# Kernel tuning notes

Measured on AMD Instinct MI355X. Metric: run time of the kernel, lower is better.

## Reference

```python
import jax, jax.numpy as jnp
import numpy as np

N_NODES = 100000
N_EDGES = 1600000
IN_CH = 128
HID = 128
OUT_CH = 64
NUM_GRAPHS = 64


def glorot(key, shape):
    lim = float(np.sqrt(6.0 / (shape[0] + shape[1])))
    return jax.random.uniform(key, shape, jnp.float32, -lim, lim)


def setup_inputs() -> dict:
    key = jax.random.key(0)
    ks = jax.random.split(key, 12)
    x = jax.random.normal(ks[0], (N_NODES, IN_CH), jnp.float32)
    edge_index = jax.random.randint(ks[1], (2, N_EDGES), 0, N_NODES, jnp.int64)
    batch = jax.random.randint(ks[2], (N_NODES,), 0, NUM_GRAPHS, jnp.int64)
    return {
        "x": x,
        "edge_index": edge_index,
        "batch": batch,
        "W1": glorot(ks[3], (IN_CH, HID)), "b1": jnp.zeros((HID,), jnp.float32),
        "W2": glorot(ks[4], (HID, HID)), "b2": jnp.zeros((HID,), jnp.float32),
        "W3": glorot(ks[5], (HID, HID)), "b3": jnp.zeros((HID,), jnp.float32),
        "Wp": glorot(ks[6], (HID, OUT_CH)), "bp": jnp.zeros((OUT_CH,), jnp.float32),
    }


def gcn_conv(x, W, b, src, dst, norm_edge, self_norm):
    # h = X W + b ; out = scatter_add(norm * h[src] -> dst) + self_loop term
    h = x @ W + b
    msg = h[src] * norm_edge[:, None]            # [E, d]
    agg = jax.ops.segment_sum(msg, dst, num_segments=N_NODES)
    return agg + h * self_norm[:, None]


def reference(x, edge_index, batch, W1, b1, W2, b2, W3, b3, Wp, bp):
    src, dst = edge_index[0], edge_index[1]
    # symmetric normalization with self-loops: deg = in-degree + 1
    deg = jax.ops.segment_sum(jnp.ones((N_EDGES,), x.dtype), dst, num_segments=N_NODES) + 1.0
    dinv = jax.lax.rsqrt(deg)
    norm_edge = dinv[src] * dinv[dst]            # [E]
    self_norm = dinv * dinv                      # [N] (self-loop weight)

    h = jax.nn.relu(gcn_conv(x, W1, b1, src, dst, norm_edge, self_norm))
    h = jax.nn.relu(gcn_conv(h, W2, b2, src, dst, norm_edge, self_norm))
    h = gcn_conv(h, W3, b3, src, dst, norm_edge, self_norm)

    # global mean pool over graphs
    sums = jax.ops.segment_sum(h, batch, num_segments=NUM_GRAPHS)
    counts = jax.ops.segment_sum(jnp.ones((N_NODES,), h.dtype), batch, num_segments=NUM_GRAPHS)
    pooled = sums / jnp.maximum(counts, 1.0)[:, None]   # [G, HID]
    return pooled @ Wp + bp                               # [G, OUT_CH]
```

## Files before the change

kernel.cpp:

```cpp
#include <hip/hip_runtime.h>

#define N_NODES 100000
#define N_EDGES 1600000
#define CH      128
#define OUT_CH  64
#define NUM_G   64
#define NREP    8

typedef unsigned short ushort_t;
typedef unsigned int uint_t;
typedef __attribute__((ext_vector_type(8))) short short8;
typedef __attribute__((ext_vector_type(4))) float f32x4;

#define WB 64
#define EB 6250
#define EB8 782
#define GB ((N_NODES + 63) / 64)
#define GB2 ((N_NODES + 127) / 128)
#define AB ((N_NODES + 3) / 4)
#define SB 98

__device__ __forceinline__ ushort_t f2b(float f) {
    union { float f; uint_t i; } v; v.f = f;
    uint_t u = v.i;
    uint_t r = (u + 0x7fffu + ((u >> 16) & 1u)) >> 16;
    return (ushort_t)r;
}
__device__ __forceinline__ float blo(uint_t u) {
    union { uint_t i; float f; } v; v.i = u << 16; return v.f;
}
__device__ __forceinline__ float bhi(uint_t u) {
    union { uint_t i; float f; } v; v.i = u & 0xffff0000u; return v.f;
}

__global__ __launch_bounds__(256) void prep_kernel(const float* __restrict__ W1,
                                                   const float* __restrict__ W2,
                                                   const float* __restrict__ W3,
                                                   ushort_t* __restrict__ Wt1,
                                                   ushort_t* __restrict__ Wt2,
                                                   ushort_t* __restrict__ Wt3,
                                                   const int* __restrict__ dst,
                                                   int* __restrict__ cnt8,
                                                   int* __restrict__ pos) {
    int b = blockIdx.x, tid = threadIdx.x;
    if (b < EB) {
        int e = b * 256 + tid;
        if (e < N_EDGES) {
            int r = b & (NREP - 1);
            pos[e] = atomicAdd(&cnt8[(size_t)r * N_NODES + dst[e]], 1);
        }
    } else {
        int wi = (b - EB) / WB;
        const float* W  = (wi == 0) ? W1 : (wi == 1) ? W2 : W3;
        ushort_t*   Wt = (wi == 0) ? Wt1 : (wi == 1) ? Wt2 : Wt3;
        int t = ((b - EB) % WB) * 256 + tid;
        int k = t >> 7, n = t & 127;
        Wt[(size_t)n * CH + k] = f2b(W[t]);
    }
}

__device__ __forceinline__ int wave_incl_scan(int v, int lane) {
#pragma unroll
    for (int off = 1; off < 64; off <<= 1) {
        int t = __shfl_up(v, off);
        if (lane >= off) v += t;
    }
    return v;
}

__global__ __launch_bounds__(1024) void scan_p1(int* __restrict__ cnt8,
                                                int* __restrict__ ptr,
                                                int* __restrict__ bsum,
                                                float* __restrict__ dinv,
                                                const int* __restrict__ batch,
                                                int* __restrict__ counts) {
    __shared__ int s_w[16];
    __shared__ int s_c[NUM_G];
    int tid = threadIdx.x, lane = tid & 63, wid = tid >> 6;
    int i = blockIdx.x * 1024 + tid;
    int v = 0;
    if (i < N_NODES) {
        int run = 0;
#pragma unroll
        for (int r = 0; r < NREP; ++r) {
            size_t idx = (size_t)r * N_NODES + i;
            int t = cnt8[idx];
            cnt8[idx] = run;
            run += t;
        }
        v = run;
        dinv[i] = rsqrtf((float)v + 1.0f);
    }
    int incl = wave_incl_scan(v, lane);
    if (lane == 63) s_w[wid] = incl;
    if (tid < NUM_G) s_c[tid] = 0;
    __syncthreads();
    if (tid < 16) {
        int w = s_w[tid];
#pragma unroll
        for (int off = 1; off < 16; off <<= 1) {
            int t = __shfl_up(w, off);
            if (tid >= off) w += t;
        }
        s_w[tid] = w;
    }
    if (i < N_NODES) atomicAdd(&s_c[batch[i]], 1);
    __syncthreads();
    int woff = (wid > 0) ? s_w[wid - 1] : 0;
    if (i < N_NODES) ptr[i] = woff + incl - v;
    if (tid == 0) bsum[blockIdx.x] = s_w[15];
    if (tid < NUM_G) atomicAdd(&counts[tid], s_c[tid]);
}

__global__ __launch_bounds__(128) void scan_p2(const int* __restrict__ bsum,
                                               int* __restrict__ boff,
                                               int* __restrict__ ptr) {
    __shared__ int s_w[2];
    int tid = threadIdx.x, lane = tid & 63, wid = tid >> 6;
    int v = (tid < SB) ? bsum[tid] : 0;
    int incl = wave_incl_scan(v, lane);
    if (lane == 63) s_w[wid] = incl;
    __syncthreads();
    int woff = (wid == 1) ? s_w[0] : 0;
    int excl = woff + incl - v;
    if (tid < SB) boff[tid] = excl;
    if (tid == SB - 1) ptr[N_NODES] = excl + v;
}

__global__ __launch_bounds__(1024) void scan_p3(int* __restrict__ ptr,
                                                const int* __restrict__ boff,
                                                int* __restrict__ cnt8) {
    int i = blockIdx.x * 1024 + threadIdx.x;
    if (i < N_NODES) {
        int fp = ptr[i] + boff[blockIdx.x];
        ptr[i] = fp;
#pragma unroll
        for (int r = 0; r < NREP; ++r)
            cnt8[(size_t)r * N_NODES + i] += fp;
    }
}

template <bool F32A>
__device__ __forceinline__ void gemm_body(int bid, int tid,
                                          const void* __restrict__ A,
                                          const ushort_t* __restrict__ Wt,
                                          const float* __restrict__ bias,
                                          ushort_t* __restrict__ H) {
    int wv = tid >> 6, lane = tid & 63;
    int q = lane >> 4, ml = lane & 15;
    int r0 = bid * 64 + wv * 16;
    int arow = r0 + ml;
    if (arow >= N_NODES) arow = N_NODES - 1;

    f32x4 acc[8];
#pragma unroll
    for (int ct = 0; ct < 8; ++ct) { acc[ct][0] = 0.f; acc[ct][1] = 0.f; acc[ct][2] = 0.f; acc[ct][3] = 0.f; }

#pragma unroll
    for (int ks = 0; ks < 4; ++ks) {
        short8 af;
        if constexpr (F32A) {
            const float* ap = (const float*)A + (size_t)arow * CH + ks * 32 + q * 8;
            f32x4 v0 = *(const f32x4*)ap;
            f32x4 v1 = *(const f32x4*)(ap + 4);
#pragma unroll
            for (int j = 0; j < 4; ++j) {
                af[j]     = (short)f2b(v0[j]);
                af[j + 4] = (short)f2b(v1[j]);
            }
        } else {
            const ushort_t* ap = (const ushort_t*)A + (size_t)arow * CH + ks * 32 + q * 8;
            af = *(const short8*)ap;
        }
#pragma unroll
        for (int ct = 0; ct < 8; ++ct) {
            short8 bf = *(const short8*)(Wt + (size_t)(ct * 16 + ml) * CH + ks * 32 + q * 8);
            acc[ct] = __builtin_amdgcn_mfma_f32_16x16x32_bf16(af, bf, acc[ct], 0, 0, 0);
        }
    }

#pragma unroll
    for (int ct = 0; ct < 8; ++ct) {
        int col = ct * 16 + ml;
        float bv = bias[col];
#pragma unroll
        for (int i = 0; i < 4; ++i) {
            int rr = r0 + q * 4 + i;
            if (rr < N_NODES)
                H[(size_t)rr * CH + col] = f2b(acc[ct][i] + bv);
        }
    }
}

__global__ __launch_bounds__(256) void fill_gemm1(const int* __restrict__ src,
                                                  const int* __restrict__ dst,
                                                  const int* __restrict__ pos,
                                                  const int* __restrict__ cnt8,
                                                  int* __restrict__ csr_src,
                                                  const float* __restrict__ x,
                                                  const ushort_t* __restrict__ Wt,
                                                  const float* __restrict__ bias,
                                                  ushort_t* __restrict__ H) {
    if (blockIdx.x < EB8) {
        int e = (blockIdx.x * 256 + threadIdx.x) * 8;
        if (e < N_EDGES) {
            const int* base = cnt8 + (size_t)((e >> 8) & (NREP - 1)) * N_NODES;
            int4 da = *(const int4*)(dst + e);
            int4 db = *(const int4*)(dst + e + 4);
            int4 pa = *(const int4*)(pos + e);
            int4 pb = *(const int4*)(pos + e + 4);
            int4 sa = *(const int4*)(src + e);
            int4 sb = *(const int4*)(src + e + 4);
            csr_src[base[da.x] + pa.x] = sa.x;
            csr_src[base[da.y] + pa.y] = sa.y;
            csr_src[base[da.z] + pa.z] = sa.z;
            csr_src[base[da.w] + pa.w] = sa.w;
            csr_src[base[db.x] + pb.x] = sb.x;
            csr_src[base[db.y] + pb.y] = sb.y;
            csr_src[base[db.z] + pb.z] = sb.z;
            csr_src[base[db.w] + pb.w] = sb.w;
        }
    } else {
        gemm_body<true>(blockIdx.x - EB8, threadIdx.x, x, Wt, bias, H);
    }
}

__global__ __launch_bounds__(512) void gemm_mfma(const ushort_t* __restrict__ A,
                                                 const ushort_t* __restrict__ Wt,
                                                 const float* __restrict__ bias,
                                                 ushort_t* __restrict__ H) {
    __shared__ ushort_t sW[CH * CH];
    int tid = threadIdx.x;
    for (int i = tid; i < CH * CH / 8; i += 512) {
        int row = i >> 4, slot = i & 15;
        uint4 v = *(const uint4*)(Wt + (size_t)row * CH + slot * 8);
        *(uint4*)(&sW[row * CH + ((slot ^ (row & 7)) * 8)]) = v;
    }
    __syncthreads();

    int wv = tid >> 6, lane = tid & 63;
    int q = lane >> 4, ml = lane & 15;
    int r0 = blockIdx.x * 128 + wv * 16;
    int arow = r0 + ml;
    if (arow >= N_NODES) arow = N_NODES - 1;
    const ushort_t* ap = A + (size_t)arow * CH;

    f32x4 acc[8];
#pragma unroll
    for (int ct = 0; ct < 8; ++ct) { acc[ct][0] = 0.f; acc[ct][1] = 0.f; acc[ct][2] = 0.f; acc[ct][3] = 0.f; }

#pragma unroll
    for (int ks = 0; ks < 4; ++ks) {
        short8 af = *(const short8*)(ap + ks * 32 + q * 8);
        int slot = ks * 4 + q;
#pragma unroll
        for (int ct = 0; ct < 8; ++ct) {
            int srow = ct * 16 + ml;
            short8 bf = *(const short8*)(&sW[srow * CH + ((slot ^ (srow & 7)) * 8)]);
            acc[ct] = __builtin_amdgcn_mfma_f32_16x16x32_bf16(af, bf, acc[ct], 0, 0, 0);
        }
    }

#pragma unroll
    for (int ct = 0; ct < 8; ++ct) {
        int col = ct * 16 + ml;
        float bv = bias[col];
#pragma unroll
        for (int i = 0; i < 4; ++i) {
            int rr = r0 + q * 4 + i;
            if (rr < N_NODES)
                H[(size_t)rr * CH + col] = f2b(acc[ct][i] + bv);
        }
    }
}

__device__ __forceinline__ void agg_node(int node, int lane, int q, int c8,
                                         const ushort_t* __restrict__ h,
                                         const int* __restrict__ csr_src,
                                         const int* __restrict__ ptr,
                                         const float* __restrict__ dinv,
                                         float (&acc)[8]) {
    int beg = ptr[node], end = ptr[node + 1];
#pragma unroll
    for (int i = 0; i < 8; ++i) acc[i] = 0.0f;

    for (int e0 = beg; e0 < end; e0 += 64) {
        int e = e0 + lane;
        int s = 0; float w = 0.0f;
        if (e < end) { s = csr_src[e]; w = dinv[s]; }
        int m = min(64, end - e0);
        for (int j0 = 0; j0 < m; j0 += 4) {
            int   sj = __shfl(s, j0 + q);
            float wj = __shfl(w, j0 + q);
            uint4 u = *(const uint4*)(h + (size_t)sj * CH + c8);
            acc[0] = fmaf(wj, blo(u.x), acc[0]);
            acc[1] = fmaf(wj, bhi(u.x), acc[1]);
            acc[2] = fmaf(wj, blo(u.y), acc[2]);
            acc[3] = fmaf(wj, bhi(u.y), acc[3]);
            acc[4] = fmaf(wj, blo(u.z), acc[4]);
            acc[5] = fmaf(wj, bhi(u.z), acc[5]);
            acc[6] = fmaf(wj, blo(u.w), acc[6]);
            acc[7] = fmaf(wj, bhi(u.w), acc[7]);
        }
    }

#pragma unroll
    for (int i = 0; i < 8; ++i) {
        acc[i] += __shfl_xor(acc[i], 16);
        acc[i] += __shfl_xor(acc[i], 32);
    }

    float dn = dinv[node];
    uint4 us = *(const uint4*)(h + (size_t)node * CH + c8);
    acc[0] = dn * fmaf(dn, blo(us.x), acc[0]);
    acc[1] = dn * fmaf(dn, bhi(us.x), acc[1]);
    acc[2] = dn * fmaf(dn, blo(us.y), acc[2]);
    acc[3] = dn * fmaf(dn, bhi(us.y), acc[3]);
    acc[4] = dn * fmaf(dn, blo(us.z), acc[4]);
    acc[5] = dn * fmaf(dn, bhi(us.z), acc[5]);
    acc[6] = dn * fmaf(dn, blo(us.w), acc[6]);
    acc[7] = dn * fmaf(dn, bhi(us.w), acc[7]);
}

__global__ __launch_bounds__(256) void agg_bf16(const ushort_t* __restrict__ h,
                                                const int* __restrict__ csr_src,
                                                const int* __restrict__ ptr,
                                                const float* __restrict__ dinv,
                                                ushort_t* __restrict__ outp) {
    int wv = threadIdx.x >> 6, lane = threadIdx.x & 63;
    int node = blockIdx.x * 4 + wv;
    if (node >= N_NODES) return;
    int q = lane >> 4;
    int c8 = (lane & 15) * 8;

    float acc[8];
    agg_node(node, lane, q, c8, h, csr_src, ptr, dinv, acc);

#pragma unroll
    for (int i = 0; i < 8; ++i) acc[i] = fmaxf(acc[i], 0.0f);

    if (q == 0) {
        uint4 o;
        o.x = (uint_t)f2b(acc[0]) | ((uint_t)f2b(acc[1]) << 16);
        o.y = (uint_t)f2b(acc[2]) | ((uint_t)f2b(acc[3]) << 16);
        o.z = (uint_t)f2b(acc[4]) | ((uint_t)f2b(acc[5]) << 16);
        o.w = (uint_t)f2b(acc[6]) | ((uint_t)f2b(acc[7]) << 16);
        *(uint4*)(outp + (size_t)node * CH + c8) = o;
    }
}

__global__ __launch_bounds__(256) void agg_pool(const ushort_t* __restrict__ h,
                                                const int* __restrict__ csr_src,
                                                const int* __restrict__ ptr,
                                                const float* __restrict__ dinv,
                                                const int* __restrict__ batch,
                                                float* __restrict__ gsums) {
    int wv = threadIdx.x >> 6, lane = threadIdx.x & 63;
    int node = blockIdx.x * 4 + wv;
    if (node >= N_NODES) return;
    int q = lane >> 4;
    int c8 = (lane & 15) * 8;

    float acc[8];
    agg_node(node, lane, q, c8, h, csr_src, ptr, dinv, acc);

    int g = batch[node];
    int jb = q * 2;
    float* bp = gsums + (size_t)(blockIdx.x & (NREP - 1)) * (NUM_G * CH)
                      + g * CH + c8 + jb;
    unsafeAtomicAdd(&bp[0], acc[jb]);
    unsafeAtomicAdd(&bp[1], acc[jb + 1]);
}

__global__ __launch_bounds__(128) void out_kernel(const float* __restrict__ gsums,
                                                  const int* __restrict__ counts,
                                                  const float* __restrict__ Wp,
                                                  const float* __restrict__ bp,
                                                  float* __restrict__ outp) {
    __shared__ float s_m[CH];
    int g = blockIdx.x, c = threadIdx.x;

    float acc = 0.0f;
#pragma unroll
    for (int r = 0; r < NREP; ++r)
        acc += gsums[(size_t)r * (NUM_G * CH) + g * CH + c];

    float inv = 1.0f / fmaxf((float)counts[g], 1.0f);
    s_m[c] = acc * inv;
    __syncthreads();

    if (c < OUT_CH) {
        float o = bp[c];
        for (int k = 0; k < CH; ++k)
            o = fmaf(s_m[k], Wp[k * OUT_CH + c], o);
        outp[g * OUT_CH + c] = o;
    }
}

extern "C" void kernel_launch(void* const* d_in, const int* in_sizes, int n_in,
                              void* d_out, int out_size, void* d_ws, size_t ws_size,
                              hipStream_t stream) {
    (void)in_sizes; (void)n_in; (void)out_size; (void)ws_size;
    const float* x     = (const float*)d_in[0];
    const int*   ei    = (const int*)d_in[1];
    const int*   batch = (const int*)d_in[2];
    const float* W1 = (const float*)d_in[3];
    const float* b1 = (const float*)d_in[4];
    const float* W2 = (const float*)d_in[5];
    const float* b2 = (const float*)d_in[6];
    const float* W3 = (const float*)d_in[7];
    const float* b3 = (const float*)d_in[8];
    const float* Wp = (const float*)d_in[9];
    const float* bp = (const float*)d_in[10];
    float* outp = (float*)d_out;

    const int* srcp = ei;
    const int* dstp = ei + N_EDGES;

    char* ws = (char*)d_ws;
    auto carve = [&](size_t bytes) {
        char* p = ws;
        ws += (bytes + 255) & ~(size_t)255;
        return p;
    };
    ushort_t* Hb = (ushort_t*)carve((size_t)N_NODES * CH * 2);
    ushort_t* Ab = (ushort_t*)carve((size_t)N_NODES * CH * 2);
    ushort_t* Wt1 = (ushort_t*)carve((size_t)CH * CH * 2);
    ushort_t* Wt2 = (ushort_t*)carve((size_t)CH * CH * 2);
    ushort_t* Wt3 = (ushort_t*)carve((size_t)CH * CH * 2);
    int*   csr_src  = (int*)carve((size_t)N_EDGES * 4);
    int*   pos      = (int*)carve((size_t)N_EDGES * 4);
    int*   cnt8     = (int*)carve((size_t)NREP * N_NODES * 4);
    int*   ptrA     = (int*)carve((size_t)(N_NODES + 1) * 4);
    float* dinv     = (float*)carve((size_t)N_NODES * 4);
    int*   bsum     = (int*)carve((size_t)SB * 4);
    int*   boff     = (int*)carve((size_t)SB * 4);
    float* gsums    = (float*)carve((size_t)NREP * NUM_G * CH * 4);
    int*   counts   = (int*)carve((size_t)NUM_G * 4);

    hipMemsetAsync(cnt8,   0, (size_t)NREP * N_NODES * 4, stream);
    hipMemsetAsync(gsums,  0, (size_t)NREP * NUM_G * CH * 4, stream);
    hipMemsetAsync(counts, 0, (size_t)NUM_G * 4, stream);

    prep_kernel<<<EB + 3 * WB, 256, 0, stream>>>(W1, W2, W3, Wt1, Wt2, Wt3,
                                                 dstp, cnt8, pos);
    scan_p1<<<SB, 1024, 0, stream>>>(cnt8, ptrA, bsum, dinv, batch, counts);
    scan_p2<<<1, 128, 0, stream>>>(bsum, boff, ptrA);
    scan_p3<<<SB, 1024, 0, stream>>>(ptrA, boff, cnt8);

    fill_gemm1<<<EB8 + GB, 256, 0, stream>>>(srcp, dstp, pos, cnt8, csr_src,
                                             x, Wt1, b1, Hb);
    agg_bf16 <<<AB, 256, 0, stream>>>(Hb, csr_src, ptrA, dinv, Ab);
    gemm_mfma<<<GB2, 512, 0, stream>>>(Ab, Wt2, b2, Hb);
    agg_bf16 <<<AB, 256, 0, stream>>>(Hb, csr_src, ptrA, dinv, Ab);
    gemm_mfma<<<GB2, 512, 0, stream>>>(Ab, Wt3, b3, Hb);
    agg_pool <<<AB, 256, 0, stream>>>(Hb, csr_src, ptrA, dinv, batch, gsums);

    out_kernel<<<NUM_G, 128, 0, stream>>>(gsums, counts, Wp, bp, outp);
}
```

Baseline: 532.2 us.

## Fuse aggregation with following GEMM and software-pipeline neighbor row loads

```diff
diff --git a/kernel.cpp b/kernel.cpp
--- a/kernel.cpp
+++ b/kernel.cpp
@@ -16,7 +16,6 @@
 #define EB 6250
 #define EB8 782
 #define GB ((N_NODES + 63) / 64)
-#define GB2 ((N_NODES + 127) / 128)
 #define AB ((N_NODES + 3) / 4)
 #define SB 98
 
@@ -225,55 +224,6 @@
     }
 }
 
-__global__ __launch_bounds__(512) void gemm_mfma(const ushort_t* __restrict__ A,
-                                                 const ushort_t* __restrict__ Wt,
-                                                 const float* __restrict__ bias,
-                                                 ushort_t* __restrict__ H) {
-    __shared__ ushort_t sW[CH * CH];
-    int tid = threadIdx.x;
-    for (int i = tid; i < CH * CH / 8; i += 512) {
-        int row = i >> 4, slot = i & 15;
-        uint4 v = *(const uint4*)(Wt + (size_t)row * CH + slot * 8);
-        *(uint4*)(&sW[row * CH + ((slot ^ (row & 7)) * 8)]) = v;
-    }
-    __syncthreads();
-
-    int wv = tid >> 6, lane = tid & 63;
-    int q = lane >> 4, ml = lane & 15;
-    int r0 = blockIdx.x * 128 + wv * 16;
-    int arow = r0 + ml;
-    if (arow >= N_NODES) arow = N_NODES - 1;
-    const ushort_t* ap = A + (size_t)arow * CH;
-
-    f32x4 acc[8];
-#pragma unroll
-    for (int ct = 0; ct < 8; ++ct) { acc[ct][0] = 0.f; acc[ct][1] = 0.f; acc[ct][2] = 0.f; acc[ct][3] = 0.f; }
-
-#pragma unroll
-    for (int ks = 0; ks < 4; ++ks) {
-        short8 af = *(const short8*)(ap + ks * 32 + q * 8);
-        int slot = ks * 4 + q;
-#pragma unroll
-        for (int ct = 0; ct < 8; ++ct) {
-            int srow = ct * 16 + ml;
-            short8 bf = *(const short8*)(&sW[srow * CH + ((slot ^ (srow & 7)) * 8)]);
-            acc[ct] = __builtin_amdgcn_mfma_f32_16x16x32_bf16(af, bf, acc[ct], 0, 0, 0);
-        }
-    }
-
-#pragma unroll
-    for (int ct = 0; ct < 8; ++ct) {
-        int col = ct * 16 + ml;
-        float bv = bias[col];
-#pragma unroll
-        for (int i = 0; i < 4; ++i) {
-            int rr = r0 + q * 4 + i;
-            if (rr < N_NODES)
-                H[(size_t)rr * CH + col] = f2b(acc[ct][i] + bv);
-        }
-    }
-}
-
 __device__ __forceinline__ void agg_node(int node, int lane, int q, int c8,
                                          const ushort_t* __restrict__ h,
                                          const int* __restrict__ csr_src,
@@ -281,6 +231,8 @@
                                          const float* __restrict__ dinv,
                                          float (&acc)[8]) {
     int beg = ptr[node], end = ptr[node + 1];
+    float dn = dinv[node];
+    uint4 us = *(const uint4*)(h + (size_t)node * CH + c8);
 #pragma unroll
     for (int i = 0; i < 8; ++i) acc[i] = 0.0f;
 
@@ -289,10 +241,18 @@
         int s = 0; float w = 0.0f;
         if (e < end) { s = csr_src[e]; w = dinv[s]; }
         int m = min(64, end - e0);
+
+        int   sj = __shfl(s, q);
+        float wj = __shfl(w, q);
+        uint4 u  = *(const uint4*)(h + (size_t)sj * CH + c8);
+
         for (int j0 = 0; j0 < m; j0 += 4) {
-            int   sj = __shfl(s, j0 + q);
-            float wj = __shfl(w, j0 + q);
-            uint4 u = *(const uint4*)(h + (size_t)sj * CH + c8);
+            uint4 un = u; float wn = 0.0f;
+            if (j0 + 4 < m) {
+                int sn = __shfl(s, j0 + 4 + q);
+                wn = __shfl(w, j0 + 4 + q);
+                un = *(const uint4*)(h + (size_t)sn * CH + c8);
+            }
             acc[0] = fmaf(wj, blo(u.x), acc[0]);
             acc[1] = fmaf(wj, bhi(u.x), acc[1]);
             acc[2] = fmaf(wj, blo(u.y), acc[2]);
@@ -301,6 +261,7 @@
             acc[5] = fmaf(wj, bhi(u.z), acc[5]);
             acc[6] = fmaf(wj, blo(u.w), acc[6]);
             acc[7] = fmaf(wj, bhi(u.w), acc[7]);
+            u = un; wj = wn;
         }
     }
 
@@ -310,8 +271,6 @@
         acc[i] += __shfl_xor(acc[i], 32);
     }
 
-    float dn = dinv[node];
-    uint4 us = *(const uint4*)(h + (size_t)node * CH + c8);
     acc[0] = dn * fmaf(dn, blo(us.x), acc[0]);
     acc[1] = dn * fmaf(dn, bhi(us.x), acc[1]);
     acc[2] = dn * fmaf(dn, blo(us.y), acc[2]);
@@ -322,30 +281,64 @@
     acc[7] = dn * fmaf(dn, bhi(us.w), acc[7]);
 }
 
-__global__ __launch_bounds__(256) void agg_bf16(const ushort_t* __restrict__ h,
+__global__ __launch_bounds__(256) void agg_gemm(const ushort_t* __restrict__ h,
                                                 const int* __restrict__ csr_src,
                                                 const int* __restrict__ ptr,
                                                 const float* __restrict__ dinv,
-                                                ushort_t* __restrict__ outp) {
-    int wv = threadIdx.x >> 6, lane = threadIdx.x & 63;
-    int node = blockIdx.x * 4 + wv;
-    if (node >= N_NODES) return;
-    int q = lane >> 4;
-    int c8 = (lane & 15) * 8;
-
-    float acc[8];
-    agg_node(node, lane, q, c8, h, csr_src, ptr, dinv, acc);
-
-#pragma unroll
-    for (int i = 0; i < 8; ++i) acc[i] = fmaxf(acc[i], 0.0f);
-
-    if (q == 0) {
-        uint4 o;
-        o.x = (uint_t)f2b(acc[0]) | ((uint_t)f2b(acc[1]) << 16);
-        o.y = (uint_t)f2b(acc[2]) | ((uint_t)f2b(acc[3]) << 16);
-        o.z = (uint_t)f2b(acc[4]) | ((uint_t)f2b(acc[5]) << 16);
-        o.w = (uint_t)f2b(acc[6]) | ((uint_t)f2b(acc[7]) << 16);
-        *(uint4*)(outp + (size_t)node * CH + c8) = o;
+                                                const ushort_t* __restrict__ Wt,
+                                                const float* __restrict__ bias,
+                                                ushort_t* __restrict__ H) {
+    __shared__ ushort_t sA[64 * CH];
+    int tid = threadIdx.x;
+    int wv = tid >> 6, lane = tid & 63;
+    int q = lane >> 4, ml = lane & 15;
+    int c8 = ml * 8;
+    int r0 = blockIdx.x * 64 + wv * 16;
+
+    for (int i = 0; i < 16; ++i) {
+        int node = r0 + i;
+        if (node >= N_NODES) break;
+        float acc[8];
+        agg_node(node, lane, q, c8, h, csr_src, ptr, dinv, acc);
+#pragma unroll
+        for (int t = 0; t < 8; ++t) acc[t] = fmaxf(acc[t], 0.0f);
+        if (q == 0) {
+            uint4 o;
+            o.x = (uint_t)f2b(acc[0]) | ((uint_t)f2b(acc[1]) << 16);
+            o.y = (uint_t)f2b(acc[2]) | ((uint_t)f2b(acc[3]) << 16);
+            o.z = (uint_t)f2b(acc[4]) | ((uint_t)f2b(acc[5]) << 16);
+            o.w = (uint_t)f2b(acc[6]) | ((uint_t)f2b(acc[7]) << 16);
+            int row = wv * 16 + i;
+            *(uint4*)(&sA[row * CH + ((ml ^ (i & 7)) * 8)]) = o;
+        }
+    }
+
+    f32x4 macc[8];
+#pragma unroll
+    for (int ct = 0; ct < 8; ++ct) { macc[ct][0] = 0.f; macc[ct][1] = 0.f; macc[ct][2] = 0.f; macc[ct][3] = 0.f; }
+
+    int arow_l = wv * 16 + ml;
+#pragma unroll
+    for (int ks = 0; ks < 4; ++ks) {
+        int slot = (ks * 4 + q) ^ (ml & 7);
+        short8 af = *(const short8*)(&sA[arow_l * CH + slot * 8]);
+#pragma unroll
+        for (int ct = 0; ct < 8; ++ct) {
+            short8 bf = *(const short8*)(Wt + (size_t)(ct * 16 + ml) * CH + ks * 32 + q * 8);
+            macc[ct] = __builtin_amdgcn_mfma_f32_16x16x32_bf16(af, bf, macc[ct], 0, 0, 0);
+        }
+    }
+
+#pragma unroll
+    for (int ct = 0; ct < 8; ++ct) {
+        int col = ct * 16 + ml;
+        float bv = bias[col];
+#pragma unroll
+        for (int i = 0; i < 4; ++i) {
+            int rr = r0 + q * 4 + i;
+            if (rr < N_NODES)
+                H[(size_t)rr * CH + col] = f2b(macc[ct][i] + bv);
+        }
     }
 }
 
@@ -450,11 +443,9 @@
 
     fill_gemm1<<<EB8 + GB, 256, 0, stream>>>(srcp, dstp, pos, cnt8, csr_src,
                                              x, Wt1, b1, Hb);
-    agg_bf16 <<<AB, 256, 0, stream>>>(Hb, csr_src, ptrA, dinv, Ab);
-    gemm_mfma<<<GB2, 512, 0, stream>>>(Ab, Wt2, b2, Hb);
-    agg_bf16 <<<AB, 256, 0, stream>>>(Hb, csr_src, ptrA, dinv, Ab);
-    gemm_mfma<<<GB2, 512, 0, stream>>>(Ab, Wt3, b3, Hb);
-    agg_pool <<<AB, 256, 0, stream>>>(Hb, csr_src, ptrA, dinv, batch, gsums);
+    agg_gemm<<<GB, 256, 0, stream>>>(Hb, csr_src, ptrA, dinv, Wt2, b2, Ab);
+    agg_gemm<<<GB, 256, 0, stream>>>(Ab, csr_src, ptrA, dinv, Wt3, b3, Hb);
+    agg_pool<<<AB, 256, 0, stream>>>(Hb, csr_src, ptrA, dinv, batch, gsums);
 
     out_kernel<<<NUM_G, 128, 0, stream>>>(gsums, counts, Wp, bp, outp);
 }
```

After: 618.9 us. +16.3%, slower.

## Split aggregation across channel halves with 8 edges in flight and prefetch

Applied to the files above, without the earlier changes.

```diff
diff --git a/kernel.cpp b/kernel.cpp
--- a/kernel.cpp
+++ b/kernel.cpp
@@ -18,6 +18,7 @@
 #define GB ((N_NODES + 63) / 64)
 #define GB2 ((N_NODES + 127) / 128)
 #define AB ((N_NODES + 3) / 4)
+#define AB2 (AB * 2)
 #define SB 98
 
 __device__ __forceinline__ ushort_t f2b(float f) {
@@ -274,13 +275,15 @@
     }
 }
 
-__device__ __forceinline__ void agg_node(int node, int lane, int q, int c8,
-                                         const ushort_t* __restrict__ h,
-                                         const int* __restrict__ csr_src,
-                                         const int* __restrict__ ptr,
-                                         const float* __restrict__ dinv,
-                                         float (&acc)[8]) {
+__device__ __forceinline__ void agg_node_h(int node, int lane, int cg, int cb,
+                                           const ushort_t* __restrict__ h,
+                                           const int* __restrict__ csr_src,
+                                           const int* __restrict__ ptr,
+                                           const float* __restrict__ dinv,
+                                           float (&acc)[8]) {
     int beg = ptr[node], end = ptr[node + 1];
+    float dn = dinv[node];
+    uint4 us = *(const uint4*)(h + (size_t)node * CH + cb);
 #pragma unroll
     for (int i = 0; i < 8; ++i) acc[i] = 0.0f;
 
@@ -289,10 +292,18 @@
         int s = 0; float w = 0.0f;
         if (e < end) { s = csr_src[e]; w = dinv[s]; }
         int m = min(64, end - e0);
-        for (int j0 = 0; j0 < m; j0 += 4) {
-            int   sj = __shfl(s, j0 + q);
-            float wj = __shfl(w, j0 + q);
-            uint4 u = *(const uint4*)(h + (size_t)sj * CH + c8);
+
+        int   sj = __shfl(s, cg);
+        float wj = __shfl(w, cg);
+        uint4 u  = *(const uint4*)(h + (size_t)sj * CH + cb);
+
+        for (int j0 = 0; j0 < m; j0 += 8) {
+            uint4 un = u; float wn = 0.0f;
+            if (j0 + 8 < m) {
+                int sn = __shfl(s, j0 + 8 + cg);
+                wn = __shfl(w, j0 + 8 + cg);
+                un = *(const uint4*)(h + (size_t)sn * CH + cb);
+            }
             acc[0] = fmaf(wj, blo(u.x), acc[0]);
             acc[1] = fmaf(wj, bhi(u.x), acc[1]);
             acc[2] = fmaf(wj, blo(u.y), acc[2]);
@@ -301,17 +312,17 @@
             acc[5] = fmaf(wj, bhi(u.z), acc[5]);
             acc[6] = fmaf(wj, blo(u.w), acc[6]);
             acc[7] = fmaf(wj, bhi(u.w), acc[7]);
+            u = un; wj = wn;
         }
     }
 
 #pragma unroll
     for (int i = 0; i < 8; ++i) {
+        acc[i] += __shfl_xor(acc[i], 8);
         acc[i] += __shfl_xor(acc[i], 16);
         acc[i] += __shfl_xor(acc[i], 32);
     }
 
-    float dn = dinv[node];
-    uint4 us = *(const uint4*)(h + (size_t)node * CH + c8);
     acc[0] = dn * fmaf(dn, blo(us.x), acc[0]);
     acc[1] = dn * fmaf(dn, bhi(us.x), acc[1]);
     acc[2] = dn * fmaf(dn, blo(us.y), acc[2]);
@@ -322,30 +333,38 @@
     acc[7] = dn * fmaf(dn, bhi(us.w), acc[7]);
 }
 
+__device__ __forceinline__ void split_decode(int b, int wv,
+                                             int& half, int& node) {
+    half = (b >> 2) & 1;
+    int nb = ((b >> 3) << 2) | (b & 3);
+    node = nb * 4 + wv;
+}
+
 __global__ __launch_bounds__(256) void agg_bf16(const ushort_t* __restrict__ h,
                                                 const int* __restrict__ csr_src,
                                                 const int* __restrict__ ptr,
                                                 const float* __restrict__ dinv,
                                                 ushort_t* __restrict__ outp) {
     int wv = threadIdx.x >> 6, lane = threadIdx.x & 63;
-    int node = blockIdx.x * 4 + wv;
+    int half, node;
+    split_decode(blockIdx.x, wv, half, node);
     if (node >= N_NODES) return;
-    int q = lane >> 4;
-    int c8 = (lane & 15) * 8;
+    int cg = lane >> 3;
+    int cb = half * 64 + (lane & 7) * 8;
 
     float acc[8];
-    agg_node(node, lane, q, c8, h, csr_src, ptr, dinv, acc);
+    agg_node_h(node, lane, cg, cb, h, csr_src, ptr, dinv, acc);
 
 #pragma unroll
     for (int i = 0; i < 8; ++i) acc[i] = fmaxf(acc[i], 0.0f);
 
-    if (q == 0) {
+    if (cg == 0) {
         uint4 o;
         o.x = (uint_t)f2b(acc[0]) | ((uint_t)f2b(acc[1]) << 16);
         o.y = (uint_t)f2b(acc[2]) | ((uint_t)f2b(acc[3]) << 16);
         o.z = (uint_t)f2b(acc[4]) | ((uint_t)f2b(acc[5]) << 16);
         o.w = (uint_t)f2b(acc[6]) | ((uint_t)f2b(acc[7]) << 16);
-        *(uint4*)(outp + (size_t)node * CH + c8) = o;
+        *(uint4*)(outp + (size_t)node * CH + cb) = o;
     }
 }
 
@@ -356,20 +375,22 @@
                                                 const int* __restrict__ batch,
                                                 float* __restrict__ gsums) {
     int wv = threadIdx.x >> 6, lane = threadIdx.x & 63;
-    int node = blockIdx.x * 4 + wv;
+    int half, node;
+    split_decode(blockIdx.x, wv, half, node);
     if (node >= N_NODES) return;
-    int q = lane >> 4;
-    int c8 = (lane & 15) * 8;
+    int cg = lane >> 3;
+    int cb = half * 64 + (lane & 7) * 8;
 
     float acc[8];
-    agg_node(node, lane, q, c8, h, csr_src, ptr, dinv, acc);
+    agg_node_h(node, lane, cg, cb, h, csr_src, ptr, dinv, acc);
+
+    float val = acc[0];
+#pragma unroll
+    for (int t = 1; t < 8; ++t) if (cg == t) val = acc[t];
 
     int g = batch[node];
-    int jb = q * 2;
-    float* bp = gsums + (size_t)(blockIdx.x & (NREP - 1)) * (NUM_G * CH)
-                      + g * CH + c8 + jb;
-    unsafeAtomicAdd(&bp[0], acc[jb]);
-    unsafeAtomicAdd(&bp[1], acc[jb + 1]);
+    unsafeAtomicAdd(gsums + (size_t)(blockIdx.x & (NREP - 1)) * (NUM_G * CH)
+                          + g * CH + cb + cg, val);
 }
 
 __global__ __launch_bounds__(128) void out_kernel(const float* __restrict__ gsums,
@@ -450,11 +471,11 @@
 
     fill_gemm1<<<EB8 + GB, 256, 0, stream>>>(srcp, dstp, pos, cnt8, csr_src,
                                              x, Wt1, b1, Hb);
-    agg_bf16 <<<AB, 256, 0, stream>>>(Hb, csr_src, ptrA, dinv, Ab);
+    agg_bf16 <<<AB2, 256, 0, stream>>>(Hb, csr_src, ptrA, dinv, Ab);
     gemm_mfma<<<GB2, 512, 0, stream>>>(Ab, Wt2, b2, Hb);
-    agg_bf16 <<<AB, 256, 0, stream>>>(Hb, csr_src, ptrA, dinv, Ab);
+    agg_bf16 <<<AB2, 256, 0, stream>>>(Hb, csr_src, ptrA, dinv, Ab);
     gemm_mfma<<<GB2, 512, 0, stream>>>(Ab, Wt3, b3, Hb);
-    agg_pool <<<AB, 256, 0, stream>>>(Hb, csr_src, ptrA, dinv, batch, gsums);
+    agg_pool <<<AB2, 256, 0, stream>>>(Hb, csr_src, ptrA, dinv, batch, gsums);
 
     out_kernel<<<NUM_G, 128, 0, stream>>>(gsums, counts, Wp, bp, outp);
 }
```

New measurement: 554.3 us. 1.04x slower.
